# Kernel optimization log

Hardware: AMD Instinct MI355X
Metric: run time of the kernel (lower is better)

The kernel has to match this reference:

```python
import jax, jax.numpy as jnp
import numpy as np

D_MODEL = 1024
NUM_HEADS = 16
D_K = D_MODEL // NUM_HEADS


def setup_inputs() -> dict:
    key = jax.random.key(0)
    ks = jax.random.split(key, 11)
    B, S, D = 2, 2048, D_MODEL
    scale = 1.0 / np.sqrt(D)
    inp = {
        'q': jax.random.normal(ks[0], (B, S, D), jnp.float32),
        'k': jax.random.normal(ks[1], (B, S, D), jnp.float32),
        'v': jax.random.normal(ks[2], (B, S, D), jnp.float32),
        'wq': jax.random.normal(ks[3], (D, D), jnp.float32) * scale,
        'bq': jnp.zeros((D,), jnp.float32),
        'wk': jax.random.normal(ks[4], (D, D), jnp.float32) * scale,
        'bk': jnp.zeros((D,), jnp.float32),
        'wv': jax.random.normal(ks[5], (D, D), jnp.float32) * scale,
        'bv': jnp.zeros((D,), jnp.float32),
        'wo': jax.random.normal(ks[6], (D, D), jnp.float32) * scale,
        'bo': jnp.zeros((D,), jnp.float32),
    }
    return inp


def _split_heads(x):
    B, S, _ = x.shape
    return x.reshape(B, S, NUM_HEADS, D_K).transpose(0, 2, 1, 3)  # [B,H,S,dk]


def reference(q, k, v, wq, bq, wk, bk, wv, bv, wo, bo):
    # Linear projections (torch Linear: x @ W^T + b)
    qh = _split_heads(q @ wq.T + bq)
    kh = _split_heads(k @ wk.T + bk)
    vh = _split_heads(v @ wv.T + bv)
    scores = jnp.einsum('bhqd,bhkd->bhqk', qh, kh) / np.sqrt(D_K)
    attn = jax.nn.softmax(scores, axis=-1)  # dropout is identity in eval
    ctx = jnp.einsum('bhqk,bhkd->bhqd', attn, vh)
    B, H, S, dk = ctx.shape
    ctx = ctx.transpose(0, 2, 1, 3).reshape(B, S, H * dk)
    return ctx @ wo.T + bo
```

## Files before the change

kernel.cpp:

```cpp
#include <hip/hip_runtime.h>
#include <hip/hip_bf16.h>
#include <math.h>

#define BATCH 2
#define SEQ   2048
#define DMODEL 1024
#define NHEAD 16
#define DK    64
#define M_TOT (BATCH*SEQ)
#define KDIM  DMODEL

typedef short bf16x8 __attribute__((ext_vector_type(8)));
typedef float f32x4  __attribute__((ext_vector_type(4)));
typedef __hip_bfloat16 bf16;

__device__ inline void gld_lds16(const void* g, void* l) {
    __builtin_amdgcn_global_load_lds(
        (const __attribute__((address_space(1))) unsigned int*)g,
        (__attribute__((address_space(3))) unsigned int*)l, 16, 0, 0);
}

__device__ inline unsigned pack2(float a, float b) {
    union { __hip_bfloat162 h; unsigned u; } t;
    t.h = __float22bfloat162_rn(make_float2(a, b));
    return t.u;
}

__global__ __launch_bounds__(256) void conv_inputs(
    const float* __restrict__ a, const float* __restrict__ b, const float* __restrict__ c,
    bf16* __restrict__ ah, bf16* __restrict__ bh, bf16* __restrict__ ch, int n)
{
    const float* src = blockIdx.y == 0 ? a : (blockIdx.y == 1 ? b : c);
    bf16* dst = blockIdx.y == 0 ? ah : (blockIdx.y == 1 ? bh : ch);
    const int i = (blockIdx.x * 256 + threadIdx.x) * 4;
    if (i < n) {
        float4 v = *(const float4*)(src + i);
        uint2 o;
        o.x = pack2(v.x, v.y);
        o.y = pack2(v.z, v.w);
        *(uint2*)(dst + i) = o;
    }
}

__global__ __launch_bounds__(256) void conv_weights(
    const float* __restrict__ wq, const float* __restrict__ wk,
    const float* __restrict__ wv, const float* __restrict__ wo,
    bf16* __restrict__ wqh, bf16* __restrict__ wkh, bf16* __restrict__ wvh,
    bf16* __restrict__ woh, bf16* __restrict__ wol, int n)
{
    const int t = blockIdx.y;
    const float* src = t == 0 ? wq : (t == 1 ? wk : (t == 2 ? wv : wo));
    bf16* dsth = t == 0 ? wqh : (t == 1 ? wkh : (t == 2 ? wvh : woh));
    const int i = (blockIdx.x * 256 + threadIdx.x) * 4;
    if (i >= n) return;
    float4 v = *(const float4*)(src + i);
    uint2 oh;
    oh.x = pack2(v.x, v.y);
    oh.y = pack2(v.z, v.w);
    *(uint2*)(dsth + i) = oh;
    if (t == 3) {
        float hx = __bfloat162float(__float2bfloat16(v.x));
        float hy = __bfloat162float(__float2bfloat16(v.y));
        float hz = __bfloat162float(__float2bfloat16(v.z));
        float hw = __bfloat162float(__float2bfloat16(v.w));
        uint2 ol;
        ol.x = pack2(v.x - hx, v.y - hy);
        ol.y = pack2(v.z - hz, v.w - hw);
        *(uint2*)(wol + i) = ol;
    }
}

template<int NSPLIT>
__global__ __launch_bounds__(256) void gemm_mfma(
    const bf16* __restrict__ Ah, const bf16* __restrict__ Al,
    const bf16* __restrict__ Wh, const bf16* __restrict__ Wl,
    const float* __restrict__ bias, void* __restrict__ out, int layout)
{
    constexpr int NP = (NSPLIT > 1) ? 2 : 1;
    __shared__ __align__(16) bf16 sA[NP][128 * 32];
    __shared__ __align__(16) bf16 sB[NP][128 * 32];

    const int tid  = threadIdx.x;
    const int wave = tid >> 6, lane = tid & 63;
    const int ln   = lane & 15, quad = lane >> 4;
    const int wm   = wave >> 1, wn = wave & 1;
    const int row0 = blockIdx.y * 128, col0 = blockIdx.x * 128;

    const int srow = lane >> 2;
    const int clog = (lane & 3) ^ (srow & 3);
    const size_t gA0 = (size_t)(row0 + wave * 16 + srow) * KDIM + clog * 8;
    const size_t gB0 = (size_t)(col0 + wave * 16 + srow) * KDIM + clog * 8;
    const int ldsoff = (wave * 16 + srow) * 64 + (lane & 3) * 16;

    const int swz = (quad ^ (ln & 3)) * 8;

    f32x4 acc[4][4] = {};

    for (int k0 = 0; k0 < KDIM; k0 += 32) {
        __syncthreads();
#pragma unroll
        for (int j = 0; j < 2; ++j) {
            const size_t go = (size_t)k0 + (size_t)j * 64 * KDIM;
            char* la = (char*)&sA[0][0] + j * 4096 + ldsoff;
            char* lb = (char*)&sB[0][0] + j * 4096 + ldsoff;
            gld_lds16(Ah + gA0 + go, la);
            gld_lds16(Wh + gB0 + go, lb);
            if (NSPLIT > 1) {
                gld_lds16(Al + gA0 + go, (char*)&sA[1][0] + j * 4096 + ldsoff);
                gld_lds16(Wl + gB0 + go, (char*)&sB[1][0] + j * 4096 + ldsoff);
            }
        }
        __syncthreads();

        bf16x8 af[4], bfr[4];
#pragma unroll
        for (int t = 0; t < 4; ++t) {
            af[t]  = *(const bf16x8*)&sA[0][(wm * 64 + t * 16 + ln) * 32 + swz];
            bfr[t] = *(const bf16x8*)&sB[0][(wn * 64 + t * 16 + ln) * 32 + swz];
        }
#pragma unroll
        for (int mt = 0; mt < 4; ++mt)
#pragma unroll
            for (int nt = 0; nt < 4; ++nt)
                acc[mt][nt] = __builtin_amdgcn_mfma_f32_16x16x32_bf16(af[mt], bfr[nt], acc[mt][nt], 0, 0, 0);

        if (NSPLIT > 1) {
            bf16x8 cf[4];
#pragma unroll
            for (int t = 0; t < 4; ++t)
                cf[t] = *(const bf16x8*)&sB[1][(wn * 64 + t * 16 + ln) * 32 + swz];
#pragma unroll
            for (int mt = 0; mt < 4; ++mt)
#pragma unroll
                for (int nt = 0; nt < 4; ++nt)
                    acc[mt][nt] = __builtin_amdgcn_mfma_f32_16x16x32_bf16(af[mt], cf[nt], acc[mt][nt], 0, 0, 0);
#pragma unroll
            for (int t = 0; t < 4; ++t)
                cf[t] = *(const bf16x8*)&sA[1][(wm * 64 + t * 16 + ln) * 32 + swz];
#pragma unroll
            for (int mt = 0; mt < 4; ++mt)
#pragma unroll
                for (int nt = 0; nt < 4; ++nt)
                    acc[mt][nt] = __builtin_amdgcn_mfma_f32_16x16x32_bf16(cf[mt], bfr[nt], acc[mt][nt], 0, 0, 0);
        }
    }

#pragma unroll
    for (int nt = 0; nt < 4; ++nt) {
        const int n = col0 + wn * 64 + nt * 16 + ln;
        const float bv = bias[n];
#pragma unroll
        for (int mt = 0; mt < 4; ++mt) {
#pragma unroll
            for (int r = 0; r < 4; ++r) {
                const int m = row0 + wm * 64 + mt * 16 + quad * 4 + r;
                const float v = acc[mt][nt][r] + bv;
                if (layout == 0) {
                    ((float*)out)[(size_t)m * DMODEL + n] = v;
                } else {
                    const int b = m >> 11, s = m & (SEQ - 1);
                    const int h = n >> 6,  d = n & (DK - 1);
                    const int bh = b * NHEAD + h;
                    bf16 hv = __float2bfloat16(v);
                    if (layout == 1)
                        ((bf16*)out)[((size_t)bh * SEQ + s) * DK + d] = hv;
                    else
                        ((bf16*)out)[((size_t)bh * DK + d) * SEQ + s] = hv;
                }
            }
        }
    }
}

#define LDP 72
__global__ __launch_bounds__(256) void flash_attn_mfma(
    const bf16* __restrict__ Q, const bf16* __restrict__ K,
    const bf16* __restrict__ Vt,
    bf16* __restrict__ ctxh, bf16* __restrict__ ctxl)
{
    __shared__ __align__(16) bf16 Ks [64 * 64];
    __shared__ __align__(16) bf16 Vts[64 * 64];
    __shared__ __align__(16) bf16 Ps [4][16 * LDP];

    const int tid  = threadIdx.x;
    const int wave = tid >> 6, lane = tid & 63;
    const int ln   = lane & 15, quad = lane >> 4;
    const int swl  = ln & 7;
    const int qt   = blockIdx.x;
    const int bh   = blockIdx.y;
    const int b    = bh >> 4, h = bh & (NHEAD - 1);

    const bf16* Qb = Q + ((size_t)bh * SEQ + qt * 64 + wave * 16) * DK;
    bf16x8 qf[2];
    qf[0] = *(const bf16x8*)(Qb + (size_t)ln * DK + 0 * 32 + quad * 8);
    qf[1] = *(const bf16x8*)(Qb + (size_t)ln * DK + 1 * 32 + quad * 8);

    f32x4 of[4] = {};
    float lp = 0.f;

    const int sr  = tid >> 2;
    const int scb = (tid & 3) * 2;
    const int ssw = sr & 7;
    const bf16* Kg0 = K  + ((size_t)bh * SEQ + sr) * DK;
    const bf16* Vg0 = Vt + ((size_t)bh * DK  + sr) * SEQ;

    for (int kt = 0; kt < SEQ / 64; ++kt) {
        __syncthreads();
        {
            const bf16* Kg = Kg0 + (size_t)kt * 64 * DK;
            const bf16* Vg = Vg0 + (size_t)kt * 64;
            uint4 k0 = *(const uint4*)(Kg + scb * 8);
            uint4 k1 = *(const uint4*)(Kg + scb * 8 + 8);
            uint4 v0 = *(const uint4*)(Vg + scb * 8);
            uint4 v1 = *(const uint4*)(Vg + scb * 8 + 8);
            *(uint4*)(&Ks [sr * 64 + ((scb    ) ^ ssw) * 8]) = k0;
            *(uint4*)(&Ks [sr * 64 + ((scb + 1) ^ ssw) * 8]) = k1;
            *(uint4*)(&Vts[sr * 64 + ((scb    ) ^ ssw) * 8]) = v0;
            *(uint4*)(&Vts[sr * 64 + ((scb + 1) ^ ssw) * 8]) = v1;
        }
        __syncthreads();

        f32x4 st[4] = {};
#pragma unroll
        for (int c = 0; c < 2; ++c) {
#pragma unroll
            for (int mt = 0; mt < 4; ++mt) {
                bf16x8 kf = *(const bf16x8*)(&Ks[(mt * 16 + ln) * 64 + ((c * 4 + quad) ^ swl) * 8]);
                st[mt] = __builtin_amdgcn_mfma_f32_16x16x32_bf16(kf, qf[c], st[mt], 0, 0, 0);
            }
        }

#pragma unroll
        for (int mt = 0; mt < 4; ++mt) {
            float p0 = __expf(st[mt][0] * 0.125f);
            float p1 = __expf(st[mt][1] * 0.125f);
            float p2 = __expf(st[mt][2] * 0.125f);
            float p3 = __expf(st[mt][3] * 0.125f);
            lp += (p0 + p1) + (p2 + p3);
            uint2 uu;
            uu.x = pack2(p0, p1);
            uu.y = pack2(p2, p3);
            *(uint2*)(&Ps[wave][ln * LDP + mt * 16 + quad * 4]) = uu;
        }

#pragma unroll
        for (int c2 = 0; c2 < 2; ++c2) {
            bf16x8 pf = *(const bf16x8*)(&Ps[wave][ln * LDP + c2 * 32 + quad * 8]);
#pragma unroll
            for (int nt = 0; nt < 4; ++nt) {
                bf16x8 vf = *(const bf16x8*)(&Vts[(nt * 16 + ln) * 64 + ((c2 * 4 + quad) ^ swl) * 8]);
                of[nt] = __builtin_amdgcn_mfma_f32_16x16x32_bf16(pf, vf, of[nt], 0, 0, 0);
            }
        }
    }

    lp += __shfl_xor(lp, 16, 64);
    lp += __shfl_xor(lp, 32, 64);
    float linv[4];
#pragma unroll
    for (int r = 0; r < 4; ++r)
        linv[r] = 1.0f / __shfl(lp, quad * 4 + r, 64);

    const size_t base = ((size_t)b * SEQ + qt * 64 + wave * 16) * DMODEL + h * DK;
#pragma unroll
    for (int nt = 0; nt < 4; ++nt)
#pragma unroll
        for (int r = 0; r < 4; ++r) {
            const float v = of[nt][r] * linv[r];
            const size_t idx = base + (size_t)(quad * 4 + r) * DMODEL + nt * 16 + ln;
            bf16 hv = __float2bfloat16(v);
            ctxh[idx] = hv;
            ctxl[idx] = __float2bfloat16(v - __bfloat162float(hv));
        }
}

extern "C" void kernel_launch(void* const* d_in, const int* in_sizes, int n_in,
                              void* d_out, int out_size, void* d_ws, size_t ws_size,
                              hipStream_t stream) {
    const float* q  = (const float*)d_in[0];
    const float* k  = (const float*)d_in[1];
    const float* v  = (const float*)d_in[2];
    const float* wq = (const float*)d_in[3];
    const float* bq = (const float*)d_in[4];
    const float* wk = (const float*)d_in[5];
    const float* bk = (const float*)d_in[6];
    const float* wv = (const float*)d_in[7];
    const float* bv = (const float*)d_in[8];
    const float* wo = (const float*)d_in[9];
    const float* bo = (const float*)d_in[10];
    float* out = (float*)d_out;

    char* ws = (char*)d_ws;
    const size_t MB = 1u << 20;
    bf16* q_hi  = (bf16*)(ws + 0 * MB);
    bf16* k_hi  = (bf16*)(ws + 8 * MB);
    bf16* v_hi  = (bf16*)(ws + 16 * MB);
    bf16* wq_hi = (bf16*)(ws + 24 * MB);
    bf16* wk_hi = (bf16*)(ws + 26 * MB);
    bf16* wv_hi = (bf16*)(ws + 28 * MB);
    bf16* wo_hi = (bf16*)(ws + 30 * MB);
    bf16* wo_lo = (bf16*)(ws + 32 * MB);
    bf16* Qp    = (bf16*)(ws + 34 * MB);
    bf16* Kp    = (bf16*)(ws + 42 * MB);
    bf16* Vpt   = (bf16*)(ws + 50 * MB);
    bf16* ctx_h = (bf16*)(ws + 0 * MB);
    bf16* ctx_l = (bf16*)(ws + 8 * MB);

    const int NX = M_TOT * DMODEL;
    const int NW = DMODEL * DMODEL;

    conv_inputs<<<dim3(NX / 1024, 3), 256, 0, stream>>>(q, k, v, q_hi, k_hi, v_hi, NX);
    conv_weights<<<dim3(NW / 1024, 4), 256, 0, stream>>>(wq, wk, wv, wo,
                                                          wq_hi, wk_hi, wv_hi, wo_hi, wo_lo, NW);

    dim3 ggrid(DMODEL / 128, M_TOT / 128);
    gemm_mfma<1><<<ggrid, 256, 0, stream>>>(q_hi, nullptr, wq_hi, nullptr, bq, Qp, 1);
    gemm_mfma<1><<<ggrid, 256, 0, stream>>>(k_hi, nullptr, wk_hi, nullptr, bk, Kp, 1);
    gemm_mfma<1><<<ggrid, 256, 0, stream>>>(v_hi, nullptr, wv_hi, nullptr, bv, Vpt, 2);

    dim3 fgrid(SEQ / 64, BATCH * NHEAD);
    flash_attn_mfma<<<fgrid, 256, 0, stream>>>(Qp, Kp, Vpt, ctx_h, ctx_l);

    gemm_mfma<3><<<ggrid, 256, 0, stream>>>(ctx_h, ctx_l, wo_hi, wo_lo, bo, out, 0);
}
```

Measured before the change: 304.1 us.

## Fuse QKV GEMMs, prescale Q for exp2, double queries per attention wave

Merges the three projection GEMMs into a single launch indexed by blockIdx.z and folds log2(e)/sqrt(dk) into the Q projection epilogue, so attention can use a raw exp2. The attention kernel now handles 32 queries per wave (128 per block), reusing each K fragment and V tile for two query tiles. K fragments are read directly from global into registers, which drops the K LDS staging. This cuts launch overhead and LDS traffic and raises arithmetic intensity, at the cost of more registers and half as many attention blocks.

```diff
diff --git a/kernel.cpp b/kernel.cpp
--- a/kernel.cpp
+++ b/kernel.cpp
@@ -13,6 +13,8 @@
 typedef short bf16x8 __attribute__((ext_vector_type(8)));
 typedef float f32x4  __attribute__((ext_vector_type(4)));
 typedef __hip_bfloat16 bf16;
+
+#define QSCALE 0.18033688011112042f
 
 __device__ inline void gld_lds16(const void* g, void* l) {
     __builtin_amdgcn_global_load_lds(
@@ -71,15 +73,12 @@
 }
 
 template<int NSPLIT>
-__global__ __launch_bounds__(256) void gemm_mfma(
+__device__ __forceinline__ void gemm_body(
     const bf16* __restrict__ Ah, const bf16* __restrict__ Al,
     const bf16* __restrict__ Wh, const bf16* __restrict__ Wl,
-    const float* __restrict__ bias, void* __restrict__ out, int layout)
-{
-    constexpr int NP = (NSPLIT > 1) ? 2 : 1;
-    __shared__ __align__(16) bf16 sA[NP][128 * 32];
-    __shared__ __align__(16) bf16 sB[NP][128 * 32];
-
+    const float* __restrict__ bias, void* __restrict__ out,
+    int layout, float scale, bf16* sA, bf16* sB)
+{
     const int tid  = threadIdx.x;
     const int wave = tid >> 6, lane = tid & 63;
     const int ln   = lane & 15, quad = lane >> 4;
@@ -101,13 +100,11 @@
 #pragma unroll
         for (int j = 0; j < 2; ++j) {
             const size_t go = (size_t)k0 + (size_t)j * 64 * KDIM;
-            char* la = (char*)&sA[0][0] + j * 4096 + ldsoff;
-            char* lb = (char*)&sB[0][0] + j * 4096 + ldsoff;
-            gld_lds16(Ah + gA0 + go, la);
-            gld_lds16(Wh + gB0 + go, lb);
+            gld_lds16(Ah + gA0 + go, (char*)sA + j * 4096 + ldsoff);
+            gld_lds16(Wh + gB0 + go, (char*)sB + j * 4096 + ldsoff);
             if (NSPLIT > 1) {
-                gld_lds16(Al + gA0 + go, (char*)&sA[1][0] + j * 4096 + ldsoff);
-                gld_lds16(Wl + gB0 + go, (char*)&sB[1][0] + j * 4096 + ldsoff);
+                gld_lds16(Al + gA0 + go, (char*)sA + 8192 + j * 4096 + ldsoff);
+                gld_lds16(Wl + gB0 + go, (char*)sB + 8192 + j * 4096 + ldsoff);
             }
         }
         __syncthreads();
@@ -115,8 +112,8 @@
         bf16x8 af[4], bfr[4];
 #pragma unroll
         for (int t = 0; t < 4; ++t) {
-            af[t]  = *(const bf16x8*)&sA[0][(wm * 64 + t * 16 + ln) * 32 + swz];
-            bfr[t] = *(const bf16x8*)&sB[0][(wn * 64 + t * 16 + ln) * 32 + swz];
+            af[t]  = *(const bf16x8*)&sA[(wm * 64 + t * 16 + ln) * 32 + swz];
+            bfr[t] = *(const bf16x8*)&sB[(wn * 64 + t * 16 + ln) * 32 + swz];
         }
 #pragma unroll
         for (int mt = 0; mt < 4; ++mt)
@@ -128,7 +125,7 @@
             bf16x8 cf[4];
 #pragma unroll
             for (int t = 0; t < 4; ++t)
-                cf[t] = *(const bf16x8*)&sB[1][(wn * 64 + t * 16 + ln) * 32 + swz];
+                cf[t] = *(const bf16x8*)&sB[4096 + (wn * 64 + t * 16 + ln) * 32 + swz];
 #pragma unroll
             for (int mt = 0; mt < 4; ++mt)
 #pragma unroll
@@ -136,7 +133,7 @@
                     acc[mt][nt] = __builtin_amdgcn_mfma_f32_16x16x32_bf16(af[mt], cf[nt], acc[mt][nt], 0, 0, 0);
 #pragma unroll
             for (int t = 0; t < 4; ++t)
-                cf[t] = *(const bf16x8*)&sA[1][(wm * 64 + t * 16 + ln) * 32 + swz];
+                cf[t] = *(const bf16x8*)&sA[4096 + (wm * 64 + t * 16 + ln) * 32 + swz];
 #pragma unroll
             for (int mt = 0; mt < 4; ++mt)
 #pragma unroll
@@ -154,7 +151,7 @@
 #pragma unroll
             for (int r = 0; r < 4; ++r) {
                 const int m = row0 + wm * 64 + mt * 16 + quad * 4 + r;
-                const float v = acc[mt][nt][r] + bv;
+                const float v = (acc[mt][nt][r] + bv) * scale;
                 if (layout == 0) {
                     ((float*)out)[(size_t)m * DMODEL + n] = v;
                 } else {
@@ -172,15 +169,41 @@
     }
 }
 
+struct QKVArgs {
+    const bf16* A[3];
+    const bf16* W[3];
+    const float* bias[3];
+    bf16* out[3];
+    float scale[3];
+    int layout[3];
+};
+
+__global__ __launch_bounds__(256) void qkv_gemm(QKVArgs a) {
+    __shared__ __align__(16) bf16 sA[128 * 32];
+    __shared__ __align__(16) bf16 sB[128 * 32];
+    const int z = blockIdx.z;
+    gemm_body<1>(a.A[z], nullptr, a.W[z], nullptr, a.bias[z],
+                 (void*)a.out[z], a.layout[z], a.scale[z], sA, sB);
+}
+
+__global__ __launch_bounds__(256) void gemm_o(
+    const bf16* __restrict__ Ah, const bf16* __restrict__ Al,
+    const bf16* __restrict__ Wh, const bf16* __restrict__ Wl,
+    const float* __restrict__ bias, float* __restrict__ out)
+{
+    __shared__ __align__(16) bf16 sA[2 * 128 * 32];
+    __shared__ __align__(16) bf16 sB[2 * 128 * 32];
+    gemm_body<3>(Ah, Al, Wh, Wl, bias, (void*)out, 0, 1.0f, sA, sB);
+}
+
 #define LDP 72
 __global__ __launch_bounds__(256) void flash_attn_mfma(
     const bf16* __restrict__ Q, const bf16* __restrict__ K,
     const bf16* __restrict__ Vt,
     bf16* __restrict__ ctxh, bf16* __restrict__ ctxl)
 {
-    __shared__ __align__(16) bf16 Ks [64 * 64];
     __shared__ __align__(16) bf16 Vts[64 * 64];
-    __shared__ __align__(16) bf16 Ps [4][16 * LDP];
+    __shared__ __align__(16) bf16 Ps[4][32 * LDP];
 
     const int tid  = threadIdx.x;
     const int wave = tid >> 6, lane = tid & 63;
@@ -190,88 +213,104 @@
     const int bh   = blockIdx.y;
     const int b    = bh >> 4, h = bh & (NHEAD - 1);
 
-    const bf16* Qb = Q + ((size_t)bh * SEQ + qt * 64 + wave * 16) * DK;
-    bf16x8 qf[2];
-    qf[0] = *(const bf16x8*)(Qb + (size_t)ln * DK + 0 * 32 + quad * 8);
-    qf[1] = *(const bf16x8*)(Qb + (size_t)ln * DK + 1 * 32 + quad * 8);
-
-    f32x4 of[4] = {};
-    float lp = 0.f;
+    const int q0 = qt * 128 + wave * 32;
+    const bf16* Qb = Q + ((size_t)bh * SEQ + q0) * DK;
+    bf16x8 qf[2][2];
+#pragma unroll
+    for (int c = 0; c < 2; ++c)
+#pragma unroll
+        for (int nt = 0; nt < 2; ++nt)
+            qf[c][nt] = *(const bf16x8*)(Qb + (size_t)(nt * 16 + ln) * DK + c * 32 + quad * 8);
+
+    f32x4 of[2][4] = {};
+    float lp[2] = {0.f, 0.f};
 
     const int sr  = tid >> 2;
     const int scb = (tid & 3) * 2;
     const int ssw = sr & 7;
-    const bf16* Kg0 = K  + ((size_t)bh * SEQ + sr) * DK;
-    const bf16* Vg0 = Vt + ((size_t)bh * DK  + sr) * SEQ;
+    const bf16* Vg0 = Vt + ((size_t)bh * DK + sr) * SEQ;
+    const bf16* Kg0 = K + (size_t)bh * SEQ * DK;
 
     for (int kt = 0; kt < SEQ / 64; ++kt) {
+        bf16x8 kf[2][4];
+#pragma unroll
+        for (int c = 0; c < 2; ++c)
+#pragma unroll
+            for (int mt = 0; mt < 4; ++mt)
+                kf[c][mt] = *(const bf16x8*)(Kg0 + (size_t)(kt * 64 + mt * 16 + ln) * DK + c * 32 + quad * 8);
+
         __syncthreads();
         {
-            const bf16* Kg = Kg0 + (size_t)kt * 64 * DK;
-            const bf16* Vg = Vg0 + (size_t)kt * 64;
-            uint4 k0 = *(const uint4*)(Kg + scb * 8);
-            uint4 k1 = *(const uint4*)(Kg + scb * 8 + 8);
+            const bf16* Vg = Vg0 + kt * 64;
             uint4 v0 = *(const uint4*)(Vg + scb * 8);
             uint4 v1 = *(const uint4*)(Vg + scb * 8 + 8);
-            *(uint4*)(&Ks [sr * 64 + ((scb    ) ^ ssw) * 8]) = k0;
-            *(uint4*)(&Ks [sr * 64 + ((scb + 1) ^ ssw) * 8]) = k1;
             *(uint4*)(&Vts[sr * 64 + ((scb    ) ^ ssw) * 8]) = v0;
             *(uint4*)(&Vts[sr * 64 + ((scb + 1) ^ ssw) * 8]) = v1;
         }
         __syncthreads();
 
-        f32x4 st[4] = {};
-#pragma unroll
-        for (int c = 0; c < 2; ++c) {
-#pragma unroll
-            for (int mt = 0; mt < 4; ++mt) {
-                bf16x8 kf = *(const bf16x8*)(&Ks[(mt * 16 + ln) * 64 + ((c * 4 + quad) ^ swl) * 8]);
-                st[mt] = __builtin_amdgcn_mfma_f32_16x16x32_bf16(kf, qf[c], st[mt], 0, 0, 0);
-            }
-        }
-
-#pragma unroll
-        for (int mt = 0; mt < 4; ++mt) {
-            float p0 = __expf(st[mt][0] * 0.125f);
-            float p1 = __expf(st[mt][1] * 0.125f);
-            float p2 = __expf(st[mt][2] * 0.125f);
-            float p3 = __expf(st[mt][3] * 0.125f);
-            lp += (p0 + p1) + (p2 + p3);
-            uint2 uu;
-            uu.x = pack2(p0, p1);
-            uu.y = pack2(p2, p3);
-            *(uint2*)(&Ps[wave][ln * LDP + mt * 16 + quad * 4]) = uu;
-        }
+        f32x4 st[4][2] = {};
+#pragma unroll
+        for (int c = 0; c < 2; ++c)
+#pragma unroll
+            for (int mt = 0; mt < 4; ++mt)
+#pragma unroll
+                for (int nt = 0; nt < 2; ++nt)
+                    st[mt][nt] = __builtin_amdgcn_mfma_f32_16x16x32_bf16(kf[c][mt], qf[c][nt], st[mt][nt], 0, 0, 0);
+
+#pragma unroll
+        for (int mt = 0; mt < 4; ++mt)
+#pragma unroll
+            for (int nt = 0; nt < 2; ++nt) {
+                float p0 = __builtin_amdgcn_exp2f(st[mt][nt][0]);
+                float p1 = __builtin_amdgcn_exp2f(st[mt][nt][1]);
+                float p2 = __builtin_amdgcn_exp2f(st[mt][nt][2]);
+                float p3 = __builtin_amdgcn_exp2f(st[mt][nt][3]);
+                lp[nt] += (p0 + p1) + (p2 + p3);
+                uint2 uu;
+                uu.x = pack2(p0, p1);
+                uu.y = pack2(p2, p3);
+                *(uint2*)(&Ps[wave][(nt * 16 + ln) * LDP + mt * 16 + quad * 4]) = uu;
+            }
 
 #pragma unroll
         for (int c2 = 0; c2 < 2; ++c2) {
-            bf16x8 pf = *(const bf16x8*)(&Ps[wave][ln * LDP + c2 * 32 + quad * 8]);
+            bf16x8 pf0 = *(const bf16x8*)(&Ps[wave][(0 * 16 + ln) * LDP + c2 * 32 + quad * 8]);
+            bf16x8 pf1 = *(const bf16x8*)(&Ps[wave][(1 * 16 + ln) * LDP + c2 * 32 + quad * 8]);
 #pragma unroll
             for (int nt = 0; nt < 4; ++nt) {
                 bf16x8 vf = *(const bf16x8*)(&Vts[(nt * 16 + ln) * 64 + ((c2 * 4 + quad) ^ swl) * 8]);
-                of[nt] = __builtin_amdgcn_mfma_f32_16x16x32_bf16(pf, vf, of[nt], 0, 0, 0);
-            }
-        }
-    }
-
-    lp += __shfl_xor(lp, 16, 64);
-    lp += __shfl_xor(lp, 32, 64);
-    float linv[4];
-#pragma unroll
-    for (int r = 0; r < 4; ++r)
-        linv[r] = 1.0f / __shfl(lp, quad * 4 + r, 64);
-
-    const size_t base = ((size_t)b * SEQ + qt * 64 + wave * 16) * DMODEL + h * DK;
-#pragma unroll
-    for (int nt = 0; nt < 4; ++nt)
-#pragma unroll
-        for (int r = 0; r < 4; ++r) {
-            const float v = of[nt][r] * linv[r];
-            const size_t idx = base + (size_t)(quad * 4 + r) * DMODEL + nt * 16 + ln;
-            bf16 hv = __float2bfloat16(v);
-            ctxh[idx] = hv;
-            ctxl[idx] = __float2bfloat16(v - __bfloat162float(hv));
-        }
+                of[0][nt] = __builtin_amdgcn_mfma_f32_16x16x32_bf16(pf0, vf, of[0][nt], 0, 0, 0);
+                of[1][nt] = __builtin_amdgcn_mfma_f32_16x16x32_bf16(pf1, vf, of[1][nt], 0, 0, 0);
+            }
+        }
+    }
+
+#pragma unroll
+    for (int nt = 0; nt < 2; ++nt) {
+        lp[nt] += __shfl_xor(lp[nt], 16, 64);
+        lp[nt] += __shfl_xor(lp[nt], 32, 64);
+    }
+    float linv[2][4];
+#pragma unroll
+    for (int mtP = 0; mtP < 2; ++mtP)
+#pragma unroll
+        for (int r = 0; r < 4; ++r)
+            linv[mtP][r] = 1.0f / __shfl(lp[mtP], quad * 4 + r, 64);
+
+    const size_t base = ((size_t)b * SEQ + q0) * DMODEL + h * DK;
+#pragma unroll
+    for (int mtP = 0; mtP < 2; ++mtP)
+#pragma unroll
+        for (int nt = 0; nt < 4; ++nt)
+#pragma unroll
+            for (int r = 0; r < 4; ++r) {
+                const float v = of[mtP][nt][r] * linv[mtP][r];
+                const size_t idx = base + (size_t)(mtP * 16 + quad * 4 + r) * DMODEL + nt * 16 + ln;
+                bf16 hv = __float2bfloat16(v);
+                ctxh[idx] = hv;
+                ctxl[idx] = __float2bfloat16(v - __bfloat162float(hv));
+            }
 }
 
 extern "C" void kernel_launch(void* const* d_in, const int* in_sizes, int n_in,
@@ -313,13 +352,20 @@
     conv_weights<<<dim3(NW / 1024, 4), 256, 0, stream>>>(wq, wk, wv, wo,
                                                           wq_hi, wk_hi, wv_hi, wo_hi, wo_lo, NW);
 
-    dim3 ggrid(DMODEL / 128, M_TOT / 128);
-    gemm_mfma<1><<<ggrid, 256, 0, stream>>>(q_hi, nullptr, wq_hi, nullptr, bq, Qp, 1);
-    gemm_mfma<1><<<ggrid, 256, 0, stream>>>(k_hi, nullptr, wk_hi, nullptr, bk, Kp, 1);
-    gemm_mfma<1><<<ggrid, 256, 0, stream>>>(v_hi, nullptr, wv_hi, nullptr, bv, Vpt, 2);
-
-    dim3 fgrid(SEQ / 64, BATCH * NHEAD);
+    QKVArgs qa;
+    qa.A[0] = q_hi;  qa.A[1] = k_hi;  qa.A[2] = v_hi;
+    qa.W[0] = wq_hi; qa.W[1] = wk_hi; qa.W[2] = wv_hi;
+    qa.bias[0] = bq; qa.bias[1] = bk; qa.bias[2] = bv;
+    qa.out[0] = Qp;  qa.out[1] = Kp;  qa.out[2] = Vpt;
+    qa.scale[0] = QSCALE; qa.scale[1] = 1.0f; qa.scale[2] = 1.0f;
+    qa.layout[0] = 1; qa.layout[1] = 1; qa.layout[2] = 2;
+
+    dim3 qgrid(DMODEL / 128, M_TOT / 128, 3);
+    qkv_gemm<<<qgrid, 256, 0, stream>>>(qa);
+
+    dim3 fgrid(SEQ / 128, BATCH * NHEAD);
     flash_attn_mfma<<<fgrid, 256, 0, stream>>>(Qp, Kp, Vpt, ctx_h, ctx_l);
 
-    gemm_mfma<3><<<ggrid, 256, 0, stream>>>(ctx_h, ctx_l, wo_hi, wo_lo, bo, out, 0);
-}
+    dim3 ogrid(DMODEL / 128, M_TOT / 128);
+    gemm_o<<<ogrid, 256, 0, stream>>>(ctx_h, ctx_l, wo_hi, wo_lo, bo, out);
+}
```

After: 294.4 us. 3.2% less time.
